# Optimization experiments

Hardware: AMD Instinct MI355X
Metric: run time of the kernel (lower is better)

The kernel has to match this reference:

```python
import jax, jax.numpy as jnp
import numpy as np

B, T, C = 16, 1024, 32
PATCH_SIZE = 4
NB_PATCHES = 400
STRETCH = 8
K = PATCH_SIZE * C          # patch_size * num_channels = 128
S_MAIN = T // STRETCH       # 128 strided steps for the main layer
P_TOP = max(int(0.15 * NB_PATCHES), PATCH_SIZE - 1)  # 60 ontop patches


def setup_inputs() -> dict:
    key = jax.random.key(0)
    k0, k1, k2, k3, k4 = jax.random.split(key, 5)
    x = jax.random.normal(k0, (B, T, C), dtype=jnp.float32)
    # flattened (time*C + channel) gather indices, stand-in for the
    # precomputed random (time, channel) pairs used by tf.gather_nd
    idx_main = jax.random.randint(k1, (S_MAIN, NB_PATCHES, K), 0, T * C, dtype=jnp.int32)
    idx_top = jax.random.randint(k2, (T, P_TOP, K), 0, T * C, dtype=jnp.int32)
    W_main = jax.random.normal(k3, (S_MAIN, NB_PATCHES, K), dtype=jnp.float32) * 0.05
    b_main = jnp.zeros((S_MAIN, NB_PATCHES), dtype=jnp.float32)
    W_top = jax.random.normal(k4, (T, P_TOP, K), dtype=jnp.float32) * 0.05
    b_top = jnp.zeros((T, P_TOP), dtype=jnp.float32)
    return {"x": x, "W_main": W_main, "b_main": b_main,
            "W_top": W_top, "b_top": b_top,
            "idx_main": idx_main, "idx_top": idx_top}


def reference(x, W_main, b_main, W_top, b_top, idx_main, idx_top):
    # x: [B, T, C] -> flatten time/channel plane for gather (== gather_nd on [T, C, B])
    Bsz, Tlen, Cch = x.shape
    flat = x.reshape(Bsz, Tlen * Cch)                      # [B, T*C]
    # main strided patches: [B, S_MAIN, NB_PATCHES, K]
    Mm = jnp.take(flat, idx_main.reshape(-1), axis=1).reshape(Bsz, *idx_main.shape)
    out_main = jax.nn.leaky_relu(
        jnp.einsum('bspk,spk->bsp', Mm, W_main) + b_main, 0.3)  # [B, S_MAIN, P]
    # upsample strided steps back to full sequence (tf_repeat along time)
    stretch = Tlen // idx_main.shape[0]
    out_main = jnp.repeat(out_main, stretch, axis=1)            # [B, T, P]
    # ontop patches at every step: [B, T, P_TOP, K]
    Mt = jnp.take(flat, idx_top.reshape(-1), axis=1).reshape(Bsz, *idx_top.shape)
    out_top = jax.nn.leaky_relu(
        jnp.einsum('btpk,tpk->btp', Mt, W_top) + b_top, 0.3)    # [B, T, P_TOP]
    return jnp.concatenate([out_main, out_top], axis=-1)       # [B, T, P + P_TOP]
```

## Files before the change

### kernel.cpp

```cpp
#include <hip/hip_runtime.h>
#include <stdint.h>

#define B_SZ    16
#define T_LEN   1024
#define C_CH    32
#define TC      (T_LEN * C_CH)
#define S_MAIN  128
#define NB_P    400
#define P_TOP   60
#define OUT_CH  (NB_P + P_TOP)
#define N_MAIN  (S_MAIN * NB_P)
#define N_TOP   (T_LEN * P_TOP)
#define N_PAIRS (N_MAIN + N_TOP)

typedef float        v4f __attribute__((ext_vector_type(4)));
typedef int          v4i __attribute__((ext_vector_type(4)));
typedef unsigned int v4u __attribute__((ext_vector_type(4)));

__device__ __forceinline__ unsigned short f32_to_bf16_rne(float f) {
    unsigned int u = __float_as_uint(f);
    unsigned int r = u + 0x7fffu + ((u >> 16) & 1u);
    return (unsigned short)(r >> 16);
}

__device__ __forceinline__ float leaky(float v) {
    return (v > 0.f) ? v : 0.3f * v;
}

#if __has_builtin(__builtin_amdgcn_make_buffer_rsrc) && __has_builtin(__builtin_amdgcn_raw_buffer_load_b128)
  #define RSRC_DECL(ptr) const auto __rsrc = \
      __builtin_amdgcn_make_buffer_rsrc((void*)(ptr), (short)0, TC * 32, 0x00020000)
  #define GATHER16(voff) __builtin_bit_cast(v4u, \
      __builtin_amdgcn_raw_buffer_load_b128(__rsrc, (int)(voff), 0, 1 ))
#else
  #define RSRC_DECL(ptr) const v4u* __rsrc = (ptr)
  #define GATHER16(voff) __rsrc[(unsigned)(voff) >> 4]
#endif

__global__ __launch_bounds__(256) void transpose_pack(const float* __restrict__ x,
                                                      unsigned int* __restrict__ xb) {
    const int i = blockIdx.x * 256 + threadIdx.x;
    unsigned int u[8];
    #pragma unroll
    for (int k = 0; k < 8; ++k) {
        float v0 = x[(size_t)(2 * k)     * TC + i];
        float v1 = x[(size_t)(2 * k + 1) * TC + i];
        u[k] = (unsigned int)f32_to_bf16_rne(v0) |
               ((unsigned int)f32_to_bf16_rne(v1) << 16);
    }
    v4u a = { u[0], u[1], u[2], u[3] };
    v4u b = { u[4], u[5], u[6], u[7] };
    v4u* out = (v4u*)xb;
    out[(size_t)i * 2]     = a;
    out[(size_t)i * 2 + 1] = b;
}

__global__ __launch_bounds__(256) void patch_fused(
    const v4u*   __restrict__ xb4,
    const int*   __restrict__ idx_main,
    const float* __restrict__ W_main,
    const float* __restrict__ bm,
    const int*   __restrict__ idx_top,
    const float* __restrict__ W_top,
    const float* __restrict__ bt,
    float*       __restrict__ ws_main,
    float*       __restrict__ out)
{
    const int wave = threadIdx.x >> 6;
    const int lane = threadIdx.x & 63;
    const int pair = blockIdx.x * 4 + wave;
    const int j    = lane >> 1;
    const int bh   = lane & 1;

    const bool is_main = (pair < N_MAIN);
    const int  q       = is_main ? pair : (pair - N_MAIN);
    const int*   idx  = is_main ? idx_main : idx_top;
    const float* W    = is_main ? W_main   : W_top;
    const float* bias = is_main ? bm       : bt;

    RSRC_DECL(xb4);

    const v4i iv = __builtin_nontemporal_load((const v4i*)(idx + (size_t)q * 128) + j);
    const v4f wv = __builtin_nontemporal_load((const v4f*)(W   + (size_t)q * 128) + j);

    float acc[8];
    #pragma unroll
    for (int k = 0; k < 8; ++k) acc[k] = 0.f;

    const int   ixs[4] = { iv.x, iv.y, iv.z, iv.w };
    const float wts[4] = { wv.x, wv.y, wv.z, wv.w };
    const int   bhofs  = bh << 4;
    #pragma unroll
    for (int m = 0; m < 4; ++m) {
        const v4u gv = GATHER16((ixs[m] << 5) | bhofs);
        const float wt = wts[m];
        acc[0] += __uint_as_float(gv.x << 16)         * wt;
        acc[1] += __uint_as_float(gv.x & 0xffff0000u) * wt;
        acc[2] += __uint_as_float(gv.y << 16)         * wt;
        acc[3] += __uint_as_float(gv.y & 0xffff0000u) * wt;
        acc[4] += __uint_as_float(gv.z << 16)         * wt;
        acc[5] += __uint_as_float(gv.z & 0xffff0000u) * wt;
        acc[6] += __uint_as_float(gv.w << 16)         * wt;
        acc[7] += __uint_as_float(gv.w & 0xffff0000u) * wt;
    }

    #pragma unroll
    for (int m = 2; m <= 32; m <<= 1)
        #pragma unroll
        for (int k = 0; k < 8; ++k)
            acc[k] += __shfl_xor(acc[k], m);

    if (j == 0) {
        const float bv = bias[q];
        if (is_main) {
            const int row = q / NB_P;
            const int p   = q - row * NB_P;
            #pragma unroll
            for (int k = 0; k < 8; ++k) {
                const int b = bh * 8 + k;
                __builtin_nontemporal_store(
                    leaky(acc[k] + bv),
                    &ws_main[((size_t)b * S_MAIN + row) * NB_P + p]);
            }
        } else {
            const int row = q / P_TOP;
            const int p   = q - row * P_TOP;
            #pragma unroll
            for (int k = 0; k < 8; ++k) {
                const int b = bh * 8 + k;
                __builtin_nontemporal_store(
                    leaky(acc[k] + bv),
                    &out[((size_t)b * T_LEN + row) * OUT_CH + NB_P + p]);
            }
        }
    }
}

__global__ __launch_bounds__(256) void upsample_main(const float* __restrict__ ws_main,
                                                     float* __restrict__ out) {
    const int o4 = blockIdx.x * 256 + threadIdx.x;
    const int row = o4 / 100;
    const int col = o4 - row * 100;
    const int b = row >> 10;
    const int t = row & 1023;
    const int s = t >> 3;
    const v4f v = ((const v4f*)ws_main)[((size_t)b * S_MAIN + s) * 100 + col];
    ((v4f*)out)[(size_t)row * 115 + col] = v;
}

extern "C" void kernel_launch(void* const* d_in, const int* in_sizes, int n_in,
                              void* d_out, int out_size, void* d_ws, size_t ws_size,
                              hipStream_t stream) {
    const float* x      = (const float*)d_in[0];
    const float* W_main = (const float*)d_in[1];
    const float* b_main = (const float*)d_in[2];
    const float* W_top  = (const float*)d_in[3];
    const float* b_top  = (const float*)d_in[4];
    const int*  idx_main = (const int*)d_in[5];
    const int*  idx_top  = (const int*)d_in[6];
    float* out = (float*)d_out;

    unsigned int* xb   = (unsigned int*)d_ws;
    float* ws_main     = (float*)((char*)d_ws + (size_t)TC * 16 * 2);

    transpose_pack<<<TC / 256, 256, 0, stream>>>(x, xb);

    patch_fused<<<N_PAIRS / 4, 256, 0, stream>>>(
        (const v4u*)xb, idx_main, W_main, b_main, idx_top, W_top, b_top,
        ws_main, out);

    upsample_main<<<(B_SZ * T_LEN * 100) / 256, 256, 0, stream>>>(ws_main, out);
}
```

Measured before the change: 249.8 us.

## Make patch kernel persistent with grid-stride loop and prefetch next indices/weights

The patch kernel moves from one wave per (step, patch) pair to a fixed grid of 2048 blocks that loop over pairs in a grid stride. Each iteration issues the index and weight loads for its next pair before gathering for the current one, so those loads overlap the dependent gather. Launch bounds now request 6 blocks per CU, and the output stores change from nontemporal to normal stores. The risk is tail imbalance and extra register pressure from holding the prefetched vectors.

```diff
diff --git a/kernel.cpp b/kernel.cpp
--- a/kernel.cpp
+++ b/kernel.cpp
@@ -12,6 +12,8 @@
 #define N_MAIN  (S_MAIN * NB_P)
 #define N_TOP   (T_LEN * P_TOP)
 #define N_PAIRS (N_MAIN + N_TOP)
+#define NBLK    2048
+#define NW      (NBLK * 4)
 
 typedef float        v4f __attribute__((ext_vector_type(4)));
 typedef int          v4i __attribute__((ext_vector_type(4)));
@@ -55,7 +57,7 @@
     out[(size_t)i * 2 + 1] = b;
 }
 
-__global__ __launch_bounds__(256) void patch_fused(
+__global__ __launch_bounds__(256, 6) void patch_fused(
     const v4u*   __restrict__ xb4,
     const int*   __restrict__ idx_main,
     const float* __restrict__ W_main,
@@ -68,71 +70,87 @@
 {
     const int wave = threadIdx.x >> 6;
     const int lane = threadIdx.x & 63;
-    const int pair = blockIdx.x * 4 + wave;
     const int j    = lane >> 1;
     const int bh   = lane & 1;
-
-    const bool is_main = (pair < N_MAIN);
-    const int  q       = is_main ? pair : (pair - N_MAIN);
-    const int*   idx  = is_main ? idx_main : idx_top;
-    const float* W    = is_main ? W_main   : W_top;
-    const float* bias = is_main ? bm       : bt;
+    const int bhofs = bh << 4;
 
     RSRC_DECL(xb4);
 
-    const v4i iv = __builtin_nontemporal_load((const v4i*)(idx + (size_t)q * 128) + j);
-    const v4f wv = __builtin_nontemporal_load((const v4f*)(W   + (size_t)q * 128) + j);
+    int pair = blockIdx.x * 4 + wave;
+    {
+    }
+    bool m_cur = (pair < N_MAIN);
+    int  q_cur = m_cur ? pair : (pair - N_MAIN);
+    v4i iv = __builtin_nontemporal_load(
+        (const v4i*)((m_cur ? idx_main : idx_top) + (size_t)q_cur * 128) + j);
+    v4f wv = __builtin_nontemporal_load(
+        (const v4f*)((m_cur ? W_main : W_top) + (size_t)q_cur * 128) + j);
 
-    float acc[8];
-    #pragma unroll
-    for (int k = 0; k < 8; ++k) acc[k] = 0.f;
+    while (pair < N_PAIRS) {
+        const int pn = pair + NW;
+        v4i ivn = iv;
+        v4f wvn = wv;
+        if (pn < N_PAIRS) {
+            const bool mn = (pn < N_MAIN);
+            const int  qn = mn ? pn : (pn - N_MAIN);
+            ivn = __builtin_nontemporal_load(
+                (const v4i*)((mn ? idx_main : idx_top) + (size_t)qn * 128) + j);
+            wvn = __builtin_nontemporal_load(
+                (const v4f*)((mn ? W_main : W_top) + (size_t)qn * 128) + j);
+        }
 
-    const int   ixs[4] = { iv.x, iv.y, iv.z, iv.w };
-    const float wts[4] = { wv.x, wv.y, wv.z, wv.w };
-    const int   bhofs  = bh << 4;
-    #pragma unroll
-    for (int m = 0; m < 4; ++m) {
-        const v4u gv = GATHER16((ixs[m] << 5) | bhofs);
-        const float wt = wts[m];
-        acc[0] += __uint_as_float(gv.x << 16)         * wt;
-        acc[1] += __uint_as_float(gv.x & 0xffff0000u) * wt;
-        acc[2] += __uint_as_float(gv.y << 16)         * wt;
-        acc[3] += __uint_as_float(gv.y & 0xffff0000u) * wt;
-        acc[4] += __uint_as_float(gv.z << 16)         * wt;
-        acc[5] += __uint_as_float(gv.z & 0xffff0000u) * wt;
-        acc[6] += __uint_as_float(gv.w << 16)         * wt;
-        acc[7] += __uint_as_float(gv.w & 0xffff0000u) * wt;
-    }
+        float acc[8];
+        #pragma unroll
+        for (int k = 0; k < 8; ++k) acc[k] = 0.f;
 
-    #pragma unroll
-    for (int m = 2; m <= 32; m <<= 1)
+        const int   ixs[4] = { iv.x, iv.y, iv.z, iv.w };
+        const float wts[4] = { wv.x, wv.y, wv.z, wv.w };
         #pragma unroll
-        for (int k = 0; k < 8; ++k)
-            acc[k] += __shfl_xor(acc[k], m);
+        for (int m = 0; m < 4; ++m) {
+            const v4u gv = GATHER16((ixs[m] << 5) | bhofs);
+            const float wt = wts[m];
+            acc[0] += __uint_as_float(gv.x << 16)         * wt;
+            acc[1] += __uint_as_float(gv.x & 0xffff0000u) * wt;
+            acc[2] += __uint_as_float(gv.y << 16)         * wt;
+            acc[3] += __uint_as_float(gv.y & 0xffff0000u) * wt;
+            acc[4] += __uint_as_float(gv.z << 16)         * wt;
+            acc[5] += __uint_as_float(gv.z & 0xffff0000u) * wt;
+            acc[6] += __uint_as_float(gv.w << 16)         * wt;
+            acc[7] += __uint_as_float(gv.w & 0xffff0000u) * wt;
+        }
 
-    if (j == 0) {
-        const float bv = bias[q];
-        if (is_main) {
-            const int row = q / NB_P;
-            const int p   = q - row * NB_P;
+        #pragma unroll
+        for (int m = 2; m <= 32; m <<= 1)
             #pragma unroll
-            for (int k = 0; k < 8; ++k) {
-                const int b = bh * 8 + k;
-                __builtin_nontemporal_store(
-                    leaky(acc[k] + bv),
-                    &ws_main[((size_t)b * S_MAIN + row) * NB_P + p]);
-            }
-        } else {
-            const int row = q / P_TOP;
-            const int p   = q - row * P_TOP;
-            #pragma unroll
-            for (int k = 0; k < 8; ++k) {
-                const int b = bh * 8 + k;
-                __builtin_nontemporal_store(
-                    leaky(acc[k] + bv),
-                    &out[((size_t)b * T_LEN + row) * OUT_CH + NB_P + p]);
+            for (int k = 0; k < 8; ++k)
+                acc[k] += __shfl_xor(acc[k], m);
+
+        if (j == 0) {
+            const bool im = (pair < N_MAIN);
+            const int  q  = im ? pair : (pair - N_MAIN);
+            const float bv = im ? bm[q] : bt[q];
+            if (im) {
+                const int row = q / NB_P;
+                const int p   = q - row * NB_P;
+                #pragma unroll
+                for (int k = 0; k < 8; ++k) {
+                    const int b = bh * 8 + k;
+                    ws_main[((size_t)b * S_MAIN + row) * NB_P + p] = leaky(acc[k] + bv);
+                }
+            } else {
+                const int row = q / P_TOP;
+                const int p   = q - row * P_TOP;
+                #pragma unroll
+                for (int k = 0; k < 8; ++k) {
+                    const int b = bh * 8 + k;
+                    out[((size_t)b * T_LEN + row) * OUT_CH + NB_P + p] = leaky(acc[k] + bv);
+                }
             }
         }
+
+        pair = pn;
+        iv = ivn;
+        wv = wvn;
     }
 }
 
@@ -165,7 +183,7 @@
 
     transpose_pack<<<TC / 256, 256, 0, stream>>>(x, xb);
 
-    patch_fused<<<N_PAIRS / 4, 256, 0, stream>>>(
+    patch_fused<<<NBLK, 256, 0, stream>>>(
         (const v4u*)xb, idx_main, W_main, b_main, idx_top, W_top, b_top,
         ws_main, out);
 
```

Result: slower. 255.5 us (+2.3%).
